# Kernel optimization log

Measured on AMD Instinct MI355X. Metric: run time of the kernel, lower is better.

The kernel has to match this reference:

```python
import jax, jax.numpy as jnp
import numpy as np

EMBED = 512
HIDDEN = 512
VOCAB = 32000
NUM_LAYERS = 2
BATCH = 32
SEQ = 64


def setup_inputs() -> dict:
    key = jax.random.key(0)
    ks = jax.random.split(key, 16)
    s_in = 1.0 / np.sqrt(EMBED + HIDDEN)  # torch Linear default U(-1/sqrt(fan_in), ..)
    s_h = 1.0 / np.sqrt(HIDDEN)
    s_e = 1.0 / np.sqrt(EMBED)
    u = lambda k, shape, s: jax.random.uniform(k, shape, jnp.float32, -s, s)
    # gate weights stacked over layers; both layers have in_dim = 1024 since embed==hidden
    gw = lambda k: u(k, (NUM_LAYERS, HIDDEN, EMBED + HIDDEN), s_in)
    gb = lambda k: u(k, (NUM_LAYERS, HIDDEN), s_in)
    return {
        "features": jax.random.normal(ks[0], (BATCH, EMBED), jnp.float32),
        "captions": jax.random.randint(ks[1], (BATCH, SEQ), 0, VOCAB),
        "embedding_w": jax.random.normal(ks[2], (VOCAB, EMBED), jnp.float32),
        "Wf": gw(ks[3]), "bf": gb(ks[4]),
        "Wi": gw(ks[5]), "bi": gb(ks[6]),
        "Wc": gw(ks[7]), "bc": gb(ks[8]),
        "Wo": gw(ks[9]), "bo": gb(ks[10]),
        "out_w": u(ks[11], (VOCAB, HIDDEN), s_h),
        "out_b": u(ks[12], (VOCAB,), s_h),
        "init_h_w": u(ks[13], (HIDDEN, EMBED), s_e),
        "init_h_b": u(ks[13], (HIDDEN,), s_e),
        "init_c_w": u(ks[14], (HIDDEN, EMBED), s_e),
        "init_c_b": u(ks[14], (HIDDEN,), s_e),
    }


def reference(features, captions, embedding_w, Wf, bf, Wi, bi, Wc, bc, Wo, bo,
              out_w, out_b, init_h_w, init_h_b, init_c_w, init_c_b):
    # init hidden/cell states (same projection replicated to every layer)
    h0 = features @ init_h_w.T + init_h_b           # [B, H]
    c0 = features @ init_c_w.T + init_c_b
    h = jnp.broadcast_to(h0, (NUM_LAYERS,) + h0.shape)  # [L, B, H]
    c = jnp.broadcast_to(c0, (NUM_LAYERS,) + c0.shape)

    # embeddings for captions[:, :-1]; dropout = identity (eval mode)
    emb = embedding_w[captions[:, :-1]]             # [B, T, E]
    xs = jnp.swapaxes(emb, 0, 1)                    # [T, B, E]

    def step(carry, x_t):
        h, c = carry
        for l in range(NUM_LAYERS):
            comb = jnp.concatenate([x_t, h[l]], axis=1)  # [B, E+H]
            f_t = jax.nn.sigmoid(comb @ Wf[l].T + bf[l])
            i_t = jax.nn.sigmoid(comb @ Wi[l].T + bi[l])
            o_t = jax.nn.sigmoid(comb @ Wo[l].T + bo[l])
            c_til = jnp.tanh(comb @ Wc[l].T + bc[l])
            c_new = f_t * c[l] + i_t * c_til
            h_new = o_t * jnp.tanh(c_new)
            h = h.at[l].set(h_new)
            c = c.at[l].set(c_new)
            x_t = h_new
        logits = h[-1] @ out_w.T + out_b            # [B, V]
        return (h, c), logits

    (_, _), outs = jax.lax.scan(step, (h, c), xs)   # outs: [T, B, V]
    return jnp.swapaxes(outs, 0, 1)                 # [B, T, V]
```

## Files before the change

kernel.cpp:

```cpp
#include <hip/hip_runtime.h>
#include <hip/hip_bf16.h>

#define T_STEPS 63
#define BATCHSZ 32
#define HID 512
#define VOCAB 32000
#define HSZ (BATCHSZ * HID)

typedef __bf16 bf16x8 __attribute__((ext_vector_type(8)));
typedef float f32x4 __attribute__((ext_vector_type(4)));

__device__ __forceinline__ unsigned short f2bf(float f) {
    __hip_bfloat16 h = __float2bfloat16(f);
    return *reinterpret_cast<unsigned short*>(&h);
}
__device__ __forceinline__ float sigm(float x) { return 1.0f / (1.0f + __expf(-x)); }

__device__ __forceinline__ float4 coh16(const float* p) {
    const unsigned long long* q = reinterpret_cast<const unsigned long long*>(p);
    unsigned long long a = __hip_atomic_load(q,     __ATOMIC_RELAXED, __HIP_MEMORY_SCOPE_AGENT);
    unsigned long long b = __hip_atomic_load(q + 1, __ATOMIC_RELAXED, __HIP_MEMORY_SCOPE_AGENT);
    float4 v;
    v.x = __uint_as_float((unsigned)(a & 0xffffffffu));
    v.y = __uint_as_float((unsigned)(a >> 32));
    v.z = __uint_as_float((unsigned)(b & 0xffffffffu));
    v.w = __uint_as_float((unsigned)(b >> 32));
    return v;
}
__device__ __forceinline__ void coh_store(float* p, float v) {
    __hip_atomic_store(p, v, __ATOMIC_RELAXED, __HIP_MEMORY_SCOPE_AGENT);
}

__device__ __forceinline__ void grid_barrier(unsigned* bar, int bid, unsigned step) {
    __syncthreads();
    if (threadIdx.x == 0) {
        asm volatile("" ::: "memory");
        unsigned prev = __hip_atomic_fetch_add(&bar[(bid & 7) << 4], 1u,
                            __ATOMIC_RELAXED, __HIP_MEMORY_SCOPE_AGENT);
        if (prev == step * 32u - 1u)
            __hip_atomic_fetch_add(&bar[128], 1u,
                __ATOMIC_RELAXED, __HIP_MEMORY_SCOPE_AGENT);
        while (__hip_atomic_load(&bar[128], __ATOMIC_RELAXED,
                                 __HIP_MEMORY_SCOPE_AGENT) < step * 8u)
            __builtin_amdgcn_s_sleep(4);
        asm volatile("" ::: "memory");
    }
    __syncthreads();
}

__global__ __launch_bounds__(512, 1) void lstm_persistent(
    const float* __restrict__ feat, const int* __restrict__ caps,
    const float* __restrict__ emb,
    const float* __restrict__ Wf, const float* __restrict__ bfp,
    const float* __restrict__ Wi, const float* __restrict__ bip,
    const float* __restrict__ Wc, const float* __restrict__ bcp,
    const float* __restrict__ Wo, const float* __restrict__ bop,
    const float* __restrict__ ihw, const float* __restrict__ ihb,
    const float* __restrict__ icw, const float* __restrict__ icb,
    float* h0buf, float* h1buf, unsigned short* h1all, unsigned* bar)
{
    __shared__ float comb[32 * 1024];
    __shared__ float red[8 * 16 * 36];

    const int tid = threadIdx.x;
    const int bid = blockIdx.x;
    const int l   = bid >> 7;
    const int blk = bid & 127;
    const int j0  = blk << 2;

    const int rl  = tid & 7;
    const int seg = tid >> 3;
    const int rot = (seg >> 1) & 3;
    const int wv  = tid >> 6;
    const int gA  = rl >> 2;
    const int jl  = rl & 3;

    const float* WgA = (gA == 0) ? Wf : Wi;
    const float* WgB = (gA == 0) ? Wc : Wo;
    const float4* rowA4 = reinterpret_cast<const float4*>(
        WgA + ((size_t)((l << 9) + j0 + jl) << 10));
    const float4* rowB4 = reinterpret_cast<const float4*>(
        WgB + ((size_t)((l << 9) + j0 + jl) << 10));
    float4 w4A[4], w4B[4];
    int qe[4];
    #pragma unroll
    for (int q = 0; q < 4; ++q) {
        qe[q] = (q + rot) & 3;
        w4A[q] = rowA4[(seg << 2) + qe[q]];
        w4B[q] = rowB4[(seg << 2) + qe[q]];
    }

    float c_reg = 0.f, bf_r = 0.f, bi_r = 0.f, bc_r = 0.f, bo_r = 0.f;
    if (tid < 128) {
        const int jlc = tid >> 5, bc = tid & 31, j = j0 + jlc;
        bf_r = bfp[(l << 9) + j];
        bi_r = bip[(l << 9) + j];
        bc_r = bcp[(l << 9) + j];
        bo_r = bop[(l << 9) + j];
        const float4* fr = reinterpret_cast<const float4*>(feat + (bc << 9));
        const float4* hr = reinterpret_cast<const float4*>(ihw + ((size_t)j << 9));
        const float4* cr = reinterpret_cast<const float4*>(icw + ((size_t)j << 9));
        float sh = 0.f, sc = 0.f;
        #pragma unroll 4
        for (int k = 0; k < 128; ++k) {
            float4 f = fr[k], hv = hr[k], cv = cr[k];
            sh += f.x * hv.x + f.y * hv.y + f.z * hv.z + f.w * hv.w;
            sc += f.x * cv.x + f.y * cv.y + f.z * cv.z + f.w * cv.w;
        }
        sh += ihb[j];
        c_reg = sc + icb[j];
        float* hb = (l == 0 ? h0buf : h1buf) + HSZ;
        coh_store(&hb[(bc << 9) + j], sh);
    }
    grid_barrier(bar, bid, 1u);

    const int cg  = tid & 255;
    const int bhi = tid >> 8;

    for (int s = 0; s < 64; ++s) {
        const bool active = (l == 0) ? (s < 63) : (s >= 1);
        if (active) {
            const int t = (l == 0) ? s : (s - 1);
            const float* h0p = h0buf + (((s + 1) & 1) ? HSZ : 0);
            const float* h1p = h1buf + ((s & 1) ? HSZ : 0);

            if (cg < 128) {
                if (l == 0) {
                    #pragma unroll
                    for (int it = 0; it < 16; ++it) {
                        int b = (it << 1) + bhi;
                        int tok = caps[(b << 6) + t];
                        float4 v = *reinterpret_cast<const float4*>(
                            emb + ((size_t)tok << 9) + (cg << 2));
                        *reinterpret_cast<float4*>(&comb[((b << 8) + cg) << 2]) = v;
                    }
                } else {
                    #pragma unroll
                    for (int it = 0; it < 16; ++it) {
                        int b = (it << 1) + bhi;
                        float4 v = coh16(h0p + (b << 9) + (cg << 2));
                        *reinterpret_cast<float4*>(&comb[((b << 8) + cg) << 2]) = v;
                    }
                }
            } else {
                const float* hp = (l == 0) ? h0p : h1p;
                const int ch = cg - 128;
                #pragma unroll
                for (int it = 0; it < 16; ++it) {
                    int b = (it << 1) + bhi;
                    float4 v = coh16(hp + (b << 9) + (ch << 2));
                    *reinterpret_cast<float4*>(&comb[((b << 8) + cg) << 2]) = v;
                }
            }
            __syncthreads();

            const float4* cb4 = reinterpret_cast<const float4*>(comb);
            const float4* Aq0 = cb4 + (seg << 2) + qe[0];
            const float4* Aq1 = cb4 + (seg << 2) + qe[1];
            const float4* Aq2 = cb4 + (seg << 2) + qe[2];
            const float4* Aq3 = cb4 + (seg << 2) + qe[3];
            for (int bg = 0; bg < 8; ++bg) {
                float aA[4], aB[4];
                #pragma unroll
                for (int bi2 = 0; bi2 < 4; ++bi2) {
                    const int b = (bg << 2) + bi2;
                    float4 c0 = Aq0[b << 8], c1 = Aq1[b << 8];
                    float4 c2 = Aq2[b << 8], c3 = Aq3[b << 8];
                    aA[bi2] = w4A[0].x*c0.x + w4A[0].y*c0.y + w4A[0].z*c0.z + w4A[0].w*c0.w
                            + w4A[1].x*c1.x + w4A[1].y*c1.y + w4A[1].z*c1.z + w4A[1].w*c1.w
                            + w4A[2].x*c2.x + w4A[2].y*c2.y + w4A[2].z*c2.z + w4A[2].w*c2.w
                            + w4A[3].x*c3.x + w4A[3].y*c3.y + w4A[3].z*c3.z + w4A[3].w*c3.w;
                    aB[bi2] = w4B[0].x*c0.x + w4B[0].y*c0.y + w4B[0].z*c0.z + w4B[0].w*c0.w
                            + w4B[1].x*c1.x + w4B[1].y*c1.y + w4B[1].z*c1.z + w4B[1].w*c1.w
                            + w4B[2].x*c2.x + w4B[2].y*c2.y + w4B[2].z*c2.z + w4B[2].w*c2.w
                            + w4B[3].x*c3.x + w4B[3].y*c3.y + w4B[3].z*c3.z + w4B[3].w*c3.w;
                }
                #pragma unroll
                for (int bi2 = 0; bi2 < 4; ++bi2) {
                    aA[bi2] += __shfl_down(aA[bi2], 32, 64);
                    aB[bi2] += __shfl_down(aB[bi2], 32, 64);
                    aA[bi2] += __shfl_down(aA[bi2], 16, 64);
                    aB[bi2] += __shfl_down(aB[bi2], 16, 64);
                    aA[bi2] += __shfl_down(aA[bi2], 8, 64);
                    aB[bi2] += __shfl_down(aB[bi2], 8, 64);
                }
                if ((tid & 63) < 8) {
                    *reinterpret_cast<float4*>(
                        &red[((wv << 4) + rl) * 36 + (bg << 2)]) =
                        make_float4(aA[0], aA[1], aA[2], aA[3]);
                    *reinterpret_cast<float4*>(
                        &red[((wv << 4) + rl + 8) * 36 + (bg << 2)]) =
                        make_float4(aB[0], aB[1], aB[2], aB[3]);
                }
            }
            __syncthreads();

            if (tid < 128) {
                const int jlc = tid >> 5, bc = tid & 31, j = j0 + jlc;
                float s0 = 0.f, s1 = 0.f, s2 = 0.f, s3 = 0.f;
                #pragma unroll
                for (int w = 0; w < 8; ++w) {
                    s0 += red[((w << 4) + 0 + jlc) * 36 + bc];
                    s1 += red[((w << 4) + 4 + jlc) * 36 + bc];
                    s2 += red[((w << 4) + 8 + jlc) * 36 + bc];
                    s3 += red[((w << 4) + 12 + jlc) * 36 + bc];
                }
                float fg = sigm(s0 + bf_r), ig = sigm(s1 + bi_r);
                float ct = tanhf(s2 + bc_r), og = sigm(s3 + bo_r);
                float cn = fg * c_reg + ig * ct;
                c_reg = cn;
                float hn = og * tanhf(cn);
                if (l == 0) {
                    coh_store(&h0buf[(s & 1) * HSZ + (bc << 9) + j], hn);
                } else {
                    coh_store(&h1buf[((s + 1) & 1) * HSZ + (bc << 9) + j], hn);
                    h1all[((size_t)t * BATCHSZ + bc) * 512 + j] = f2bf(hn);
                }
            }
        }
        if (s < 63) grid_barrier(bar, bid, (unsigned)(s + 2));
    }
}

__global__ __launch_bounds__(256) void proj_gemm(
    const unsigned short* __restrict__ H, const float* __restrict__ W,
    const float* __restrict__ bias, float* __restrict__ out)
{
    __shared__ unsigned short sA[128 * 72];
    __shared__ unsigned short sB[128 * 72];
    const int tid = threadIdx.x;
    const int bm = blockIdx.x, bn = blockIdx.y;
    const int wave = tid >> 6, lane = tid & 63;
    const int wm = (wave >> 1) << 6, wn = (wave & 1) << 6;
    const int lr = lane & 15, quad = lane >> 4;

    f32x4 acc[4][4];
    #pragma unroll
    for (int i = 0; i < 4; ++i)
        #pragma unroll
        for (int j = 0; j < 4; ++j) acc[i][j] = (f32x4){0.f, 0.f, 0.f, 0.f};

    for (int k0 = 0; k0 < 512; k0 += 64) {
        __syncthreads();
        #pragma unroll
        for (int it = 0; it < 4; ++it) {
            int c = tid + (it << 8);
            int row = c >> 3, col = (c & 7) << 3;
            int gm = (bm << 7) + row;
            uint4 av = make_uint4(0u, 0u, 0u, 0u);
            if (gm < 2016)
                av = *reinterpret_cast<const uint4*>(&H[(size_t)gm * 512 + k0 + col]);
            *reinterpret_cast<uint4*>(&sA[row * 72 + col]) = av;
        }
        #pragma unroll
        for (int it = 0; it < 8; ++it) {
            int c = tid + (it << 8);
            int row = c >> 4, col = (c & 15) << 2;
            int gn = (bn << 7) + row;
            float4 bv = *reinterpret_cast<const float4*>(&W[(size_t)gn * 512 + k0 + col]);
            uint2 p;
            p.x = (unsigned int)f2bf(bv.x) | ((unsigned int)f2bf(bv.y) << 16);
            p.y = (unsigned int)f2bf(bv.z) | ((unsigned int)f2bf(bv.w) << 16);
            *reinterpret_cast<uint2*>(&sB[row * 72 + col]) = p;
        }
        __syncthreads();
        #pragma unroll
        for (int ks = 0; ks < 2; ++ks) {
            bf16x8 af[4], bg[4];
            #pragma unroll
            for (int i = 0; i < 4; ++i)
                af[i] = *reinterpret_cast<const bf16x8*>(
                    &sA[(wm + (i << 4) + lr) * 72 + (ks << 5) + (quad << 3)]);
            #pragma unroll
            for (int i = 0; i < 4; ++i)
                bg[i] = *reinterpret_cast<const bf16x8*>(
                    &sB[(wn + (i << 4) + lr) * 72 + (ks << 5) + (quad << 3)]);
            #pragma unroll
            for (int mi = 0; mi < 4; ++mi)
                #pragma unroll
                for (int ni = 0; ni < 4; ++ni)
                    acc[mi][ni] = __builtin_amdgcn_mfma_f32_16x16x32_bf16(
                        af[mi], bg[ni], acc[mi][ni], 0, 0, 0);
        }
    }

    #pragma unroll
    for (int ni = 0; ni < 4; ++ni) {
        int n = (bn << 7) + wn + (ni << 4) + lr;
        float bv = bias[n];
        #pragma unroll
        for (int mi = 0; mi < 4; ++mi) {
            #pragma unroll
            for (int r = 0; r < 4; ++r) {
                int m = (bm << 7) + wm + (mi << 4) + (quad << 2) + r;
                if (m < 2016) {
                    int b = m & 31, tt = m >> 5;
                    out[((size_t)(b * 63 + tt)) * VOCAB + n] = acc[mi][ni][r] + bv;
                }
            }
        }
    }
}

extern "C" void kernel_launch(void* const* d_in, const int* in_sizes, int n_in,
                              void* d_out, int out_size, void* d_ws, size_t ws_size,
                              hipStream_t stream) {
    const float* feat = (const float*)d_in[0];
    const int*   caps = (const int*)d_in[1];
    const float* emb  = (const float*)d_in[2];
    const float* Wf   = (const float*)d_in[3];
    const float* bfp  = (const float*)d_in[4];
    const float* Wi   = (const float*)d_in[5];
    const float* bip  = (const float*)d_in[6];
    const float* Wc   = (const float*)d_in[7];
    const float* bcp  = (const float*)d_in[8];
    const float* Wo   = (const float*)d_in[9];
    const float* bop  = (const float*)d_in[10];
    const float* Wout = (const float*)d_in[11];
    const float* bout = (const float*)d_in[12];
    const float* ihw  = (const float*)d_in[13];
    const float* ihb  = (const float*)d_in[14];
    const float* icw  = (const float*)d_in[15];
    const float* icb  = (const float*)d_in[16];

    char* ws = (char*)d_ws;
    unsigned* bar         = (unsigned*)ws;
    float* h0buf          = (float*)(ws + 1024);
    float* h1buf          = (float*)(ws + 1024 + 131072);
    unsigned short* h1all = (unsigned short*)(ws + 1024 + 262144);

    hipMemsetAsync(ws, 0, 1024, stream);

    lstm_persistent<<<dim3(256), dim3(512), 0, stream>>>(
        feat, caps, emb, Wf, bfp, Wi, bip, Wc, bcp, Wo, bop,
        ihw, ihb, icw, icb, h0buf, h1buf, h1all, bar);

    proj_gemm<<<dim3(16, 250), dim3(256), 0, stream>>>(h1all, Wout, bout,
                                                       (float*)d_out);
}
```

Before: 1.833 ms.

## Flag-array grid barrier, batch-split LSTM blocks, pipelined state loads, prefetched embeddings

The grid barrier changes from a hierarchical atomic counter to per-block flag stores that one wavefront polls in parallel. The LSTM work is repartitioned so each block handles 8 hidden units for half the batch. The comb tile shrinks and is XOR-swizzled, and state loads for the next batch chunk overlap the dot products of the current chunk. Embedding rows for the next timestep are prefetched into registers, and h1all is written in batch-major order so the projection GEMM stores rows contiguously. Risks include more per-step __syncthreads, larger weight register footprint, and the barrier flag array assuming 256 blocks.

```diff
diff --git a/kernel.cpp b/kernel.cpp
--- a/kernel.cpp
+++ b/kernel.cpp
@@ -33,16 +33,19 @@
 
 __device__ __forceinline__ void grid_barrier(unsigned* bar, int bid, unsigned step) {
     __syncthreads();
-    if (threadIdx.x == 0) {
-        asm volatile("" ::: "memory");
-        unsigned prev = __hip_atomic_fetch_add(&bar[(bid & 7) << 4], 1u,
-                            __ATOMIC_RELAXED, __HIP_MEMORY_SCOPE_AGENT);
-        if (prev == step * 32u - 1u)
-            __hip_atomic_fetch_add(&bar[128], 1u,
-                __ATOMIC_RELAXED, __HIP_MEMORY_SCOPE_AGENT);
-        while (__hip_atomic_load(&bar[128], __ATOMIC_RELAXED,
-                                 __HIP_MEMORY_SCOPE_AGENT) < step * 8u)
-            __builtin_amdgcn_s_sleep(4);
+    const int tid = threadIdx.x;
+    if (tid == 0)
+        __hip_atomic_store(&bar[bid], step, __ATOMIC_RELAXED, __HIP_MEMORY_SCOPE_AGENT);
+    if (tid < 64) {
+        const unsigned* f = bar + tid;
+        for (;;) {
+            unsigned a = __hip_atomic_load(f,       __ATOMIC_RELAXED, __HIP_MEMORY_SCOPE_AGENT);
+            unsigned b = __hip_atomic_load(f + 64,  __ATOMIC_RELAXED, __HIP_MEMORY_SCOPE_AGENT);
+            unsigned c = __hip_atomic_load(f + 128, __ATOMIC_RELAXED, __HIP_MEMORY_SCOPE_AGENT);
+            unsigned d = __hip_atomic_load(f + 192, __ATOMIC_RELAXED, __HIP_MEMORY_SCOPE_AGENT);
+            if (__all(a >= step && b >= step && c >= step && d >= step)) break;
+            __builtin_amdgcn_s_sleep(1);
+        }
         asm volatile("" ::: "memory");
     }
     __syncthreads();
@@ -59,45 +62,52 @@
     const float* __restrict__ icw, const float* __restrict__ icb,
     float* h0buf, float* h1buf, unsigned short* h1all, unsigned* bar)
 {
-    __shared__ float comb[32 * 1024];
-    __shared__ float red[8 * 16 * 36];
+    __shared__ float comb[16 * 1024];
+    __shared__ float red[8 * 32 * 20];
 
     const int tid = threadIdx.x;
     const int bid = blockIdx.x;
     const int l   = bid >> 7;
-    const int blk = bid & 127;
-    const int j0  = blk << 2;
-
-    const int rl  = tid & 7;
-    const int seg = tid >> 3;
-    const int rot = (seg >> 1) & 3;
+    const int sub = bid & 127;
+    const int j0  = (sub >> 1) << 3;
+    const int b0  = (sub & 1) << 4;
+
     const int wv  = tid >> 6;
-    const int gA  = rl >> 2;
-    const int jl  = rl & 3;
-
-    const float* WgA = (gA == 0) ? Wf : Wi;
-    const float* WgB = (gA == 0) ? Wc : Wo;
+    const int seg = (wv << 2) | ((tid >> 4) & 3);
+    const int rl  = tid & 15;
+    const int g   = rl >> 3;
+    const int u   = rl & 7;
+
+    const int cg   = tid & 255;
+    const int bhi  = tid >> 8;
+    const int slotW = cg ^ ((cg >> 3) & 7);
+    const int chOff = (cg < 128) ? cg : (cg - 128);
+
+    float4* comb4 = reinterpret_cast<float4*>(comb);
+    const float4* emb4 = reinterpret_cast<const float4*>(emb);
+
+    const float* WgA = (g == 0) ? Wf : Wi;
+    const float* WgB = (g == 0) ? Wc : Wo;
     const float4* rowA4 = reinterpret_cast<const float4*>(
-        WgA + ((size_t)((l << 9) + j0 + jl) << 10));
+        WgA + ((size_t)((l << 9) + j0 + u) << 10));
     const float4* rowB4 = reinterpret_cast<const float4*>(
-        WgB + ((size_t)((l << 9) + j0 + jl) << 10));
-    float4 w4A[4], w4B[4];
-    int qe[4];
+        WgB + ((size_t)((l << 9) + j0 + u) << 10));
+    float4 w4A[8], w4B[8];
     #pragma unroll
-    for (int q = 0; q < 4; ++q) {
-        qe[q] = (q + rot) & 3;
-        w4A[q] = rowA4[(seg << 2) + qe[q]];
-        w4B[q] = rowB4[(seg << 2) + qe[q]];
+    for (int q = 0; q < 8; ++q) {
+        w4A[q] = rowA4[(seg << 3) + q];
+        w4B[q] = rowB4[(seg << 3) + q];
     }
 
     float c_reg = 0.f, bf_r = 0.f, bi_r = 0.f, bc_r = 0.f, bo_r = 0.f;
     if (tid < 128) {
-        const int jlc = tid >> 5, bc = tid & 31, j = j0 + jlc;
+        const int uu = tid >> 4, bc = tid & 15;
+        const int j = j0 + uu, b = b0 + bc;
         bf_r = bfp[(l << 9) + j];
         bi_r = bip[(l << 9) + j];
         bc_r = bcp[(l << 9) + j];
         bo_r = bop[(l << 9) + j];
-        const float4* fr = reinterpret_cast<const float4*>(feat + (bc << 9));
+        const float4* fr = reinterpret_cast<const float4*>(feat + ((size_t)b << 9));
         const float4* hr = reinterpret_cast<const float4*>(ihw + ((size_t)j << 9));
         const float4* cr = reinterpret_cast<const float4*>(icw + ((size_t)j << 9));
         float sh = 0.f, sc = 0.f;
@@ -110,12 +120,20 @@
         sh += ihb[j];
         c_reg = sc + icb[j];
         float* hb = (l == 0 ? h0buf : h1buf) + HSZ;
-        coh_store(&hb[(bc << 9) + j], sh);
-    }
+        coh_store(&hb[((size_t)b << 9) + j], sh);
+    }
+
+    float4 pf[8];
+    if (l == 0 && cg < 128) {
+        #pragma unroll
+        for (int k = 0; k < 8; ++k) {
+            int b = b0 + (k << 1) + bhi;
+            int tok = caps[b << 6];
+            pf[k] = emb4[(size_t)tok * 128 + cg];
+        }
+    }
+
     grid_barrier(bar, bid, 1u);
-
-    const int cg  = tid & 255;
-    const int bhi = tid >> 8;
 
     for (int s = 0; s < 64; ++s) {
         const bool active = (l == 0) ? (s < 63) : (s >= 1);
@@ -123,87 +141,94 @@
             const int t = (l == 0) ? s : (s - 1);
             const float* h0p = h0buf + (((s + 1) & 1) ? HSZ : 0);
             const float* h1p = h1buf + ((s & 1) ? HSZ : 0);
-
-            if (cg < 128) {
-                if (l == 0) {
+            const bool fromPf = (l == 0 && cg < 128);
+            const float* src = (l == 0) ? h0p : ((cg < 128) ? h0p : h1p);
+
+            {
+                float4 L0, L1;
+                if (!fromPf) {
+                    L0 = coh16(src + ((size_t)(b0 + bhi)     << 9) + (chOff << 2));
+                    L1 = coh16(src + ((size_t)(b0 + 2 + bhi) << 9) + (chOff << 2));
+                }
+                if (fromPf) {
+                    comb4[(bhi)     * 256 + slotW] = pf[0];
+                    comb4[(2 + bhi) * 256 + slotW] = pf[1];
+                } else {
+                    comb4[(bhi)     * 256 + slotW] = L0;
+                    comb4[(2 + bhi) * 256 + slotW] = L1;
+                }
+            }
+            __syncthreads();
+
+            #pragma unroll
+            for (int c = 0; c < 4; ++c) {
+                float4 L0, L1;
+                if (c < 3 && !fromPf) {
+                    L0 = coh16(src + ((size_t)(b0 + 4*(c+1) + bhi)     << 9) + (chOff << 2));
+                    L1 = coh16(src + ((size_t)(b0 + 4*(c+1) + 2 + bhi) << 9) + (chOff << 2));
+                }
+                float aA[4], aB[4];
+                #pragma unroll
+                for (int bi2 = 0; bi2 < 4; ++bi2) {
+                    const float4* cb = comb4 + (4*c + bi2) * 256;
+                    float sA0 = 0.f, sA1 = 0.f, sB0 = 0.f, sB1 = 0.f;
                     #pragma unroll
-                    for (int it = 0; it < 16; ++it) {
-                        int b = (it << 1) + bhi;
-                        int tok = caps[(b << 6) + t];
-                        float4 v = *reinterpret_cast<const float4*>(
-                            emb + ((size_t)tok << 9) + (cg << 2));
-                        *reinterpret_cast<float4*>(&comb[((b << 8) + cg) << 2]) = v;
+                    for (int q = 0; q < 8; ++q) {
+                        float4 cc = cb[(seg << 3) | (q ^ (seg & 7))];
+                        sA0 += w4A[q].x*cc.x + w4A[q].y*cc.y;
+                        sA1 += w4A[q].z*cc.z + w4A[q].w*cc.w;
+                        sB0 += w4B[q].x*cc.x + w4B[q].y*cc.y;
+                        sB1 += w4B[q].z*cc.z + w4B[q].w*cc.w;
                     }
-                } else {
-                    #pragma unroll
-                    for (int it = 0; it < 16; ++it) {
-                        int b = (it << 1) + bhi;
-                        float4 v = coh16(h0p + (b << 9) + (cg << 2));
-                        *reinterpret_cast<float4*>(&comb[((b << 8) + cg) << 2]) = v;
-                    }
-                }
-            } else {
-                const float* hp = (l == 0) ? h0p : h1p;
-                const int ch = cg - 128;
-                #pragma unroll
-                for (int it = 0; it < 16; ++it) {
-                    int b = (it << 1) + bhi;
-                    float4 v = coh16(hp + (b << 9) + (ch << 2));
-                    *reinterpret_cast<float4*>(&comb[((b << 8) + cg) << 2]) = v;
-                }
-            }
-            __syncthreads();
-
-            const float4* cb4 = reinterpret_cast<const float4*>(comb);
-            const float4* Aq0 = cb4 + (seg << 2) + qe[0];
-            const float4* Aq1 = cb4 + (seg << 2) + qe[1];
-            const float4* Aq2 = cb4 + (seg << 2) + qe[2];
-            const float4* Aq3 = cb4 + (seg << 2) + qe[3];
-            for (int bg = 0; bg < 8; ++bg) {
-                float aA[4], aB[4];
+                    aA[bi2] = sA0 + sA1;
+                    aB[bi2] = sB0 + sB1;
+                }
                 #pragma unroll
                 for (int bi2 = 0; bi2 < 4; ++bi2) {
-                    const int b = (bg << 2) + bi2;
-                    float4 c0 = Aq0[b << 8], c1 = Aq1[b << 8];
-                    float4 c2 = Aq2[b << 8], c3 = Aq3[b << 8];
-                    aA[bi2] = w4A[0].x*c0.x + w4A[0].y*c0.y + w4A[0].z*c0.z + w4A[0].w*c0.w
-                            + w4A[1].x*c1.x + w4A[1].y*c1.y + w4A[1].z*c1.z + w4A[1].w*c1.w
-                            + w4A[2].x*c2.x + w4A[2].y*c2.y + w4A[2].z*c2.z + w4A[2].w*c2.w
-                            + w4A[3].x*c3.x + w4A[3].y*c3.y + w4A[3].z*c3.z + w4A[3].w*c3.w;
-                    aB[bi2] = w4B[0].x*c0.x + w4B[0].y*c0.y + w4B[0].z*c0.z + w4B[0].w*c0.w
-                            + w4B[1].x*c1.x + w4B[1].y*c1.y + w4B[1].z*c1.z + w4B[1].w*c1.w
-                            + w4B[2].x*c2.x + w4B[2].y*c2.y + w4B[2].z*c2.z + w4B[2].w*c2.w
-                            + w4B[3].x*c3.x + w4B[3].y*c3.y + w4B[3].z*c3.z + w4B[3].w*c3.w;
-                }
-                #pragma unroll
-                for (int bi2 = 0; bi2 < 4; ++bi2) {
-                    aA[bi2] += __shfl_down(aA[bi2], 32, 64);
-                    aB[bi2] += __shfl_down(aB[bi2], 32, 64);
-                    aA[bi2] += __shfl_down(aA[bi2], 16, 64);
-                    aB[bi2] += __shfl_down(aB[bi2], 16, 64);
-                    aA[bi2] += __shfl_down(aA[bi2], 8, 64);
-                    aB[bi2] += __shfl_down(aB[bi2], 8, 64);
-                }
-                if ((tid & 63) < 8) {
+                    aA[bi2] += __shfl_down(aA[bi2], 16);
+                    aB[bi2] += __shfl_down(aB[bi2], 16);
+                    aA[bi2] += __shfl_down(aA[bi2], 32);
+                    aB[bi2] += __shfl_down(aB[bi2], 32);
+                }
+                if ((tid & 63) < 16) {
                     *reinterpret_cast<float4*>(
-                        &red[((wv << 4) + rl) * 36 + (bg << 2)]) =
+                        &red[((wv << 5) + rl) * 20 + (c << 2)]) =
                         make_float4(aA[0], aA[1], aA[2], aA[3]);
                     *reinterpret_cast<float4*>(
-                        &red[((wv << 4) + rl + 8) * 36 + (bg << 2)]) =
+                        &red[((wv << 5) + rl + 16) * 20 + (c << 2)]) =
                         make_float4(aB[0], aB[1], aB[2], aB[3]);
                 }
-            }
-            __syncthreads();
+                if (c < 3) {
+                    if (fromPf) {
+                        comb4[(4*(c+1) + bhi)     * 256 + slotW] = pf[2*(c+1)];
+                        comb4[(4*(c+1) + 2 + bhi) * 256 + slotW] = pf[2*(c+1) + 1];
+                    } else {
+                        comb4[(4*(c+1) + bhi)     * 256 + slotW] = L0;
+                        comb4[(4*(c+1) + 2 + bhi) * 256 + slotW] = L1;
+                    }
+                }
+                __syncthreads();
+            }
+
+            if (l == 0 && cg < 128 && s < 62) {
+                #pragma unroll
+                for (int k = 0; k < 8; ++k) {
+                    int b = b0 + (k << 1) + bhi;
+                    int tok = caps[(b << 6) + s + 1];
+                    pf[k] = emb4[(size_t)tok * 128 + cg];
+                }
+            }
 
             if (tid < 128) {
-                const int jlc = tid >> 5, bc = tid & 31, j = j0 + jlc;
+                const int uu = tid >> 4, bc = tid & 15;
+                const int j = j0 + uu, b = b0 + bc;
                 float s0 = 0.f, s1 = 0.f, s2 = 0.f, s3 = 0.f;
                 #pragma unroll
                 for (int w = 0; w < 8; ++w) {
-                    s0 += red[((w << 4) + 0 + jlc) * 36 + bc];
-                    s1 += red[((w << 4) + 4 + jlc) * 36 + bc];
-                    s2 += red[((w << 4) + 8 + jlc) * 36 + bc];
-                    s3 += red[((w << 4) + 12 + jlc) * 36 + bc];
+                    s0 += red[((w << 5) + uu)      * 20 + bc];
+                    s1 += red[((w << 5) + 8 + uu)  * 20 + bc];
+                    s2 += red[((w << 5) + 16 + uu) * 20 + bc];
+                    s3 += red[((w << 5) + 24 + uu) * 20 + bc];
                 }
                 float fg = sigm(s0 + bf_r), ig = sigm(s1 + bi_r);
                 float ct = tanhf(s2 + bc_r), og = sigm(s3 + bo_r);
@@ -211,10 +236,10 @@
                 c_reg = cn;
                 float hn = og * tanhf(cn);
                 if (l == 0) {
-                    coh_store(&h0buf[(s & 1) * HSZ + (bc << 9) + j], hn);
+                    coh_store(&h0buf[(s & 1) * HSZ + ((size_t)b << 9) + j], hn);
                 } else {
-                    coh_store(&h1buf[((s + 1) & 1) * HSZ + (bc << 9) + j], hn);
-                    h1all[((size_t)t * BATCHSZ + bc) * 512 + j] = f2bf(hn);
+                    coh_store(&h1buf[((s + 1) & 1) * HSZ + ((size_t)b << 9) + j], hn);
+                    h1all[((size_t)b * 63 + t) * 512 + j] = f2bf(hn);
                 }
             }
         }
@@ -293,10 +318,8 @@
             #pragma unroll
             for (int r = 0; r < 4; ++r) {
                 int m = (bm << 7) + wm + (mi << 4) + (quad << 2) + r;
-                if (m < 2016) {
-                    int b = m & 31, tt = m >> 5;
-                    out[((size_t)(b * 63 + tt)) * VOCAB + n] = acc[mi][ni][r] + bv;
-                }
+                if (m < 2016)
+                    out[(size_t)m * VOCAB + n] = acc[mi][ni][r] + bv;
             }
         }
     }
```

Result: faster. 1.596 ms (-12.9%).
